# Optimization experiments

Hardware: AMD Instinct MI355X
Metric: run time of the kernel (lower is better)

The kernel has to match this reference:

```python
import jax, jax.numpy as jnp
import numpy as np

VIEW_NUM = 360
CHAN_NUM = 512
BATCH = 2
IMG = 512


def setup_inputs() -> dict:
    key = jax.random.key(0)
    x = jax.random.normal(key, (BATCH, 1, IMG, IMG), dtype=jnp.float32)
    return {"x": x}


def _bilinear_sample_zeros(img, ix, iy):
    """Bilinear sample img (B,1,H,W) at pixel coords ix, iy (H,W), zeros padding.
    Matches F.grid_sample(mode='bilinear', padding_mode='zeros', align_corners=False)."""
    H, W = img.shape[-2], img.shape[-1]
    x0 = jnp.floor(ix)
    y0 = jnp.floor(iy)
    x1 = x0 + 1.0
    y1 = y0 + 1.0
    wx1 = ix - x0
    wx0 = 1.0 - wx1
    wy1 = iy - y0
    wy0 = 1.0 - wy1

    def gather(yy, xx):
        valid = (xx >= 0) & (xx <= W - 1) & (yy >= 0) & (yy <= H - 1)
        xi = jnp.clip(xx, 0, W - 1).astype(jnp.int32)
        yi = jnp.clip(yy, 0, H - 1).astype(jnp.int32)
        # fancy-index over spatial dims -> (B,1,H,W)
        return img[:, :, yi, xi] * valid.astype(img.dtype)

    return (gather(y0, x0) * (wy0 * wx0)
            + gather(y0, x1) * (wy0 * wx1)
            + gather(y1, x0) * (wy1 * wx0)
            + gather(y1, x1) * (wy1 * wx1))


def _fp(x):
    B, C, H, W = x.shape
    # affine_grid base coords, align_corners=False: (2i+1)/N - 1
    bx = (2.0 * jnp.arange(W, dtype=x.dtype) + 1.0) / W - 1.0
    by = (2.0 * jnp.arange(H, dtype=x.dtype) + 1.0) / H - 1.0
    X = bx[None, :]  # (1,W)
    Y = by[:, None]  # (H,1)
    i = jnp.arange(VIEW_NUM, dtype=x.dtype)
    angles = -jnp.pi * (i + 1.0) / VIEW_NUM - jnp.pi
    cosv = jnp.cos(angles)
    sinv = jnp.sin(angles)

    def per_view(carry, cs):
        c, s = cs
        # theta = [[c,-s,0],[s,c,0]]; grid = base @ theta^T
        gx = c * X - s * Y  # (H,W) normalized sample x
        gy = s * X + c * Y  # (H,W) normalized sample y
        # unnormalize (align_corners=False)
        ix = ((gx + 1.0) * W - 1.0) * 0.5
        iy = ((gy + 1.0) * H - 1.0) * 0.5
        samp = _bilinear_sample_zeros(x, ix, iy)  # (B,1,H,W)
        return carry, jnp.sum(samp, axis=2)  # sum over height -> (B,1,W)

    _, cols = jax.lax.scan(per_view, 0, (cosv, sinv))  # (V,B,1,W)
    sino = jnp.transpose(cols, (1, 2, 3, 0)) * 0.5  # (B,1,chanNum,viewNum)
    return sino


def reference(x):
    return _fp(x)
```

## Files before the change

### kernel.cpp

```cpp
#include <hip/hip_runtime.h>

typedef __fp16 h2 __attribute__((ext_vector_type(2)));

constexpr int VIEWS = 360;
constexpr int IMGSZ = 512;
constexpr int BATCH = 2;
constexpr int WCHUNK = 64;
constexpr int KH = 64;
constexpr int NXF4 = 25;
constexpr int PITCH = 100;
constexpr int MAXNY = 94;
constexpr int PW = 712;
constexpr int PH = 704;
constexpr int PAD = 96;

__global__ __launch_bounds__(256) void pad_kernel(const float* __restrict__ x,
                                                  unsigned* __restrict__ padq) {
    constexpr int PW4 = PW / 4;
    constexpr int total = PH * PW4;
    int idx = blockIdx.x * 256 + threadIdx.x;
    if (idx >= total) return;
    int py = idx / PW4;
    int px4 = idx - py * PW4;
    int gx = px4 * 4 - PAD;
    int gy = py - PAD;
    const float* img0 = x;
    const float* img1 = x + (size_t)IMGSZ * IMGSZ;
    bool rowok = (unsigned)gy < (unsigned)IMGSZ;
    float4 a = make_float4(0.f, 0.f, 0.f, 0.f);
    float4 bq = a;
    if (rowok && (unsigned)gx < (unsigned)IMGSZ) {
        a  = *(const float4*)(img0 + (size_t)gy * IMGSZ + gx);
        bq = *(const float4*)(img1 + (size_t)gy * IMGSZ + gx);
    }
    uint4 d;
    d.x = __builtin_bit_cast(unsigned, __builtin_amdgcn_cvt_pkrtz(a.x, bq.x));
    d.y = __builtin_bit_cast(unsigned, __builtin_amdgcn_cvt_pkrtz(a.y, bq.y));
    d.z = __builtin_bit_cast(unsigned, __builtin_amdgcn_cvt_pkrtz(a.z, bq.z));
    d.w = __builtin_bit_cast(unsigned, __builtin_amdgcn_cvt_pkrtz(a.w, bq.w));
    *(uint4*)&padq[(size_t)idx * 4] = d;
}

__global__ __launch_bounds__(256) void fp_kernel(const unsigned* __restrict__ padq,
                                                 float* __restrict__ out) {
    __shared__ __align__(16) unsigned tileU[10240];

    int blk = blockIdx.x;
    int wc = blk & 7;
    int v = blk >> 3;

    int tid = threadIdx.x;
    int lane = tid & 63;
    int g = tid >> 6;
    int w = wc * WCHUNK + lane;

    double ang = -3.14159265358979323846 * (double)(v + 1) / (double)VIEWS
                 - 3.14159265358979323846;
    float c = (float)cos(ang);
    float s = (float)sin(ang);

    float xw = (float)w + 0.5f - 256.0f;
    float cxw = fmaf(c, xw, 255.5f);
    float sxw = fmaf(s, xw, 255.5f);

    float lo = -1e30f, hi = 1e30f;
    {
        float coef = -s, base = cxw;
        if (fabsf(coef) > 1e-6f) {
            float a = (-1.0f - base) / coef;
            float bq = (512.0f - base) / coef;
            lo = fmaxf(lo, fminf(a, bq));
            hi = fminf(hi, fmaxf(a, bq));
        } else if (!(base > -1.0f && base < 512.0f)) {
            lo = 1e30f; hi = -1e30f;
        }
    }
    {
        float coef = c, base = sxw;
        if (fabsf(coef) > 1e-6f) {
            float a = (-1.0f - base) / coef;
            float bq = (512.0f - base) / coef;
            lo = fmaxf(lo, fminf(a, bq));
            hi = fminf(hi, fmaxf(a, bq));
        } else if (!(base > -1.0f && base < 512.0f)) {
            lo = 1e30f; hi = -1e30f;
        }
    }
    float h0f = fminf(fmaxf(floorf(lo + 255.5f) - 1.0f, 0.0f), 512.0f);
    float h1f = fminf(fmaxf(ceilf(hi + 255.5f) + 1.0f, -1.0f), 511.0f);
    int h0 = (int)h0f;
    int h1 = (int)h1f;

    int bh0 = h0, bh1 = h1;
    #pragma unroll
    for (int m = 1; m < 64; m <<= 1) {
        bh0 = min(bh0, __shfl_xor(bh0, m, 64));
        bh1 = max(bh1, __shfl_xor(bh1, m, 64));
    }

    float xa = (float)(wc * WCHUNK) + 0.5f - 256.0f;
    float xb = xa + 63.0f;

    float acc0 = 0.0f, acc1 = 0.0f;
    float step4x = -4.0f * s;
    float step4y = 4.0f * c;

    for (int hc = bh0; hc <= bh1; hc += KH) {
        int hend = min(hc + KH - 1, bh1);

        float ha = (float)hc - 255.5f;
        float hb = (float)hend - 255.5f;
        float ix00 = c * xa - s * ha, ix01 = c * xa - s * hb;
        float ix10 = c * xb - s * ha, ix11 = c * xb - s * hb;
        float iy00 = s * xa + c * ha, iy01 = s * xa + c * hb;
        float iy10 = s * xb + c * ha, iy11 = s * xb + c * hb;
        float ixmn = fminf(fminf(ix00, ix01), fminf(ix10, ix11)) + 255.5f;
        float iymn = fminf(fminf(iy00, iy01), fminf(iy10, iy11)) + 255.5f;
        float iymx = fmaxf(fmaxf(iy00, iy01), fmaxf(iy10, iy11)) + 255.5f;
        int x_lo = (int)floorf(ixmn) - 1;
        int x_lo4 = x_lo & ~3;
        int y_lo = (int)floorf(iymn) - 1;
        int NY = min((int)floorf(iymx) + 3 - y_lo, MAXNY);
        int total4 = NY * NXF4;
        int nit = (total4 + 255) >> 8;

        __syncthreads();

        {
            const unsigned* pb = padq + (y_lo + PAD) * PW + (x_lo4 + PAD);
            for (int k = 0; k < nit; ++k) {
                int i = (k << 8) + tid;
                int ic = min(i, total4 - 1);
                int ry = ic / NXF4;
                uint4 val = *(const uint4*)(pb + 4 * ic + (PW - 4 * NXF4) * ry);
                *(uint4*)&tileU[i << 2] = val;
            }
        }
        __syncthreads();

        float hh0 = (float)(hc + g) - 255.5f;
        float ixr = fmaf(-s, hh0, cxw) - (float)x_lo4;
        float iyr = fmaf(c, hh0, sxw) - (float)y_lo;
        h2 accp0 = (h2)0.0f;
        h2 accp1 = (h2)0.0f;
        int parity = 0;
        #pragma unroll 4
        for (int h = hc + g; h <= hend; h += 4) {
            float fx = floorf(ixr);
            float fy = floorf(iyr);
            int lx = (int)fx;
            int ly = (int)fy;
            float wx1 = ixr - fx;
            float wy1 = iyr - fy;
            h2 wx0s = __builtin_amdgcn_cvt_pkrtz(1.0f - wx1, 1.0f - wx1);
            h2 wx1s = __builtin_amdgcn_cvt_pkrtz(wx1, wx1);
            h2 wy0s = __builtin_amdgcn_cvt_pkrtz(1.0f - wy1, 1.0f - wy1);
            h2 wy1s = __builtin_amdgcn_cvt_pkrtz(wy1, wy1);
            const unsigned* p = tileU + (ly * PITCH + lx);
            unsigned q00 = p[0];
            unsigned q01 = p[1];
            unsigned q10 = p[PITCH];
            unsigned q11 = p[PITCH + 1];
            h2 r0 = __builtin_bit_cast(h2, q00) * wx0s
                  + __builtin_bit_cast(h2, q01) * wx1s;
            h2 r1 = __builtin_bit_cast(h2, q10) * wx0s
                  + __builtin_bit_cast(h2, q11) * wx1s;
            h2 contrib = r0 * wy0s + r1 * wy1s;
            if (parity) accp1 += contrib; else accp0 += contrib;
            parity ^= 1;
            ixr += step4x;
            iyr += step4y;
        }
        acc0 += (float)accp0.x + (float)accp1.x;
        acc1 += (float)accp0.y + (float)accp1.y;
    }

    __syncthreads();
    tileU[(g << 6) + lane] = __float_as_uint(acc0);
    tileU[256 + (g << 6) + lane] = __float_as_uint(acc1);
    __syncthreads();
    if (g == 0) {
        float r0 = __uint_as_float(tileU[lane]) + __uint_as_float(tileU[64 + lane]) +
                   __uint_as_float(tileU[128 + lane]) + __uint_as_float(tileU[192 + lane]);
        float r1 = __uint_as_float(tileU[256 + lane]) + __uint_as_float(tileU[320 + lane]) +
                   __uint_as_float(tileU[384 + lane]) + __uint_as_float(tileU[448 + lane]);
        size_t o = (size_t)w * VIEWS + v;
        out[o] = r0 * 0.5f;
        out[(size_t)IMGSZ * VIEWS + o] = r1 * 0.5f;
    }
}

extern "C" void kernel_launch(void* const* d_in, const int* in_sizes, int n_in,
                              void* d_out, int out_size, void* d_ws, size_t ws_size,
                              hipStream_t stream) {
    const float* x = (const float*)d_in[0];
    float* out = (float*)d_out;
    unsigned* padq = (unsigned*)d_ws;

    constexpr int padTotal = PH * (PW / 4);
    pad_kernel<<<(padTotal + 255) / 256, 256, 0, stream>>>(x, padq);

    int nblocks = VIEWS * (IMGSZ / WCHUNK);
    fp_kernel<<<nblocks, 256, 0, stream>>>(padq, out);
}
```

Measured before the change: 159.6 us.

## Fuse padding/fp16 packing into tile load and shrink tile height

```diff
diff --git a/kernel.cpp b/kernel.cpp
--- a/kernel.cpp
+++ b/kernel.cpp
@@ -4,46 +4,15 @@
 
 constexpr int VIEWS = 360;
 constexpr int IMGSZ = 512;
-constexpr int BATCH = 2;
 constexpr int WCHUNK = 64;
-constexpr int KH = 64;
-constexpr int NXF4 = 25;
-constexpr int PITCH = 100;
-constexpr int MAXNY = 94;
-constexpr int PW = 712;
-constexpr int PH = 704;
-constexpr int PAD = 96;
+constexpr int KH = 32;
+constexpr int NXF4 = 20;
+constexpr int PITCH = 80;
+constexpr int MAXNY = 76;
 
-__global__ __launch_bounds__(256) void pad_kernel(const float* __restrict__ x,
-                                                  unsigned* __restrict__ padq) {
-    constexpr int PW4 = PW / 4;
-    constexpr int total = PH * PW4;
-    int idx = blockIdx.x * 256 + threadIdx.x;
-    if (idx >= total) return;
-    int py = idx / PW4;
-    int px4 = idx - py * PW4;
-    int gx = px4 * 4 - PAD;
-    int gy = py - PAD;
-    const float* img0 = x;
-    const float* img1 = x + (size_t)IMGSZ * IMGSZ;
-    bool rowok = (unsigned)gy < (unsigned)IMGSZ;
-    float4 a = make_float4(0.f, 0.f, 0.f, 0.f);
-    float4 bq = a;
-    if (rowok && (unsigned)gx < (unsigned)IMGSZ) {
-        a  = *(const float4*)(img0 + (size_t)gy * IMGSZ + gx);
-        bq = *(const float4*)(img1 + (size_t)gy * IMGSZ + gx);
-    }
-    uint4 d;
-    d.x = __builtin_bit_cast(unsigned, __builtin_amdgcn_cvt_pkrtz(a.x, bq.x));
-    d.y = __builtin_bit_cast(unsigned, __builtin_amdgcn_cvt_pkrtz(a.y, bq.y));
-    d.z = __builtin_bit_cast(unsigned, __builtin_amdgcn_cvt_pkrtz(a.z, bq.z));
-    d.w = __builtin_bit_cast(unsigned, __builtin_amdgcn_cvt_pkrtz(a.w, bq.w));
-    *(uint4*)&padq[(size_t)idx * 4] = d;
-}
-
-__global__ __launch_bounds__(256) void fp_kernel(const unsigned* __restrict__ padq,
+__global__ __launch_bounds__(256) void fp_kernel(const float* __restrict__ x,
                                                  float* __restrict__ out) {
-    __shared__ __align__(16) unsigned tileU[10240];
+    __shared__ __align__(16) unsigned tileU[6144];
 
     int blk = blockIdx.x;
     int wc = blk & 7;
@@ -58,6 +27,9 @@
                  - 3.14159265358979323846;
     float c = (float)cos(ang);
     float s = (float)sin(ang);
+
+    const float* __restrict__ img0 = x;
+    const float* __restrict__ img1 = x + (size_t)IMGSZ * IMGSZ;
 
     float xw = (float)w + 0.5f - 256.0f;
     float cxw = fmaf(c, xw, 255.5f);
@@ -126,15 +98,28 @@
 
         __syncthreads();
 
-        {
-            const unsigned* pb = padq + (y_lo + PAD) * PW + (x_lo4 + PAD);
-            for (int k = 0; k < nit; ++k) {
-                int i = (k << 8) + tid;
-                int ic = min(i, total4 - 1);
-                int ry = ic / NXF4;
-                uint4 val = *(const uint4*)(pb + 4 * ic + (PW - 4 * NXF4) * ry);
-                *(uint4*)&tileU[i << 2] = val;
+        for (int k = 0; k < nit; ++k) {
+            int i = (k << 8) + tid;
+            int ic = min(i, total4 - 1);
+            int ry = ic / NXF4;
+            int rx4 = ic - ry * NXF4;
+            int gy = y_lo + ry;
+            int gx = x_lo4 + (rx4 << 2);
+            bool ok = ((unsigned)gy < (unsigned)IMGSZ) &
+                      ((unsigned)gx < (unsigned)IMGSZ);
+            float4 a = make_float4(0.f, 0.f, 0.f, 0.f);
+            float4 bq = a;
+            if (ok) {
+                size_t off = (size_t)gy * IMGSZ + gx;
+                a  = *(const float4*)(img0 + off);
+                bq = *(const float4*)(img1 + off);
             }
+            uint4 d;
+            d.x = __builtin_bit_cast(unsigned, __builtin_amdgcn_cvt_pkrtz(a.x, bq.x));
+            d.y = __builtin_bit_cast(unsigned, __builtin_amdgcn_cvt_pkrtz(a.y, bq.y));
+            d.z = __builtin_bit_cast(unsigned, __builtin_amdgcn_cvt_pkrtz(a.z, bq.z));
+            d.w = __builtin_bit_cast(unsigned, __builtin_amdgcn_cvt_pkrtz(a.w, bq.w));
+            *(uint4*)&tileU[i << 2] = d;
         }
         __syncthreads();
 
@@ -152,20 +137,16 @@
             int ly = (int)fy;
             float wx1 = ixr - fx;
             float wy1 = iyr - fy;
-            h2 wx0s = __builtin_amdgcn_cvt_pkrtz(1.0f - wx1, 1.0f - wx1);
-            h2 wx1s = __builtin_amdgcn_cvt_pkrtz(wx1, wx1);
-            h2 wy0s = __builtin_amdgcn_cvt_pkrtz(1.0f - wy1, 1.0f - wy1);
-            h2 wy1s = __builtin_amdgcn_cvt_pkrtz(wy1, wy1);
+            h2 wxs = __builtin_amdgcn_cvt_pkrtz(wx1, wx1);
+            h2 wys = __builtin_amdgcn_cvt_pkrtz(wy1, wy1);
             const unsigned* p = tileU + (ly * PITCH + lx);
-            unsigned q00 = p[0];
-            unsigned q01 = p[1];
-            unsigned q10 = p[PITCH];
-            unsigned q11 = p[PITCH + 1];
-            h2 r0 = __builtin_bit_cast(h2, q00) * wx0s
-                  + __builtin_bit_cast(h2, q01) * wx1s;
-            h2 r1 = __builtin_bit_cast(h2, q10) * wx0s
-                  + __builtin_bit_cast(h2, q11) * wx1s;
-            h2 contrib = r0 * wy0s + r1 * wy1s;
+            h2 t00 = __builtin_bit_cast(h2, p[0]);
+            h2 t01 = __builtin_bit_cast(h2, p[1]);
+            h2 t10 = __builtin_bit_cast(h2, p[PITCH]);
+            h2 t11 = __builtin_bit_cast(h2, p[PITCH + 1]);
+            h2 r0 = t00 + (t01 - t00) * wxs;
+            h2 r1 = t10 + (t11 - t10) * wxs;
+            h2 contrib = r0 + (r1 - r0) * wys;
             if (parity) accp1 += contrib; else accp0 += contrib;
             parity ^= 1;
             ixr += step4x;
@@ -195,11 +176,6 @@
                               hipStream_t stream) {
     const float* x = (const float*)d_in[0];
     float* out = (float*)d_out;
-    unsigned* padq = (unsigned*)d_ws;
-
-    constexpr int padTotal = PH * (PW / 4);
-    pad_kernel<<<(padTotal + 255) / 256, 256, 0, stream>>>(x, padq);
-
     int nblocks = VIEWS * (IMGSZ / WCHUNK);
-    fp_kernel<<<nblocks, 256, 0, stream>>>(padq, out);
+    fp_kernel<<<nblocks, 256, 0, stream>>>(x, out);
 }
```

After: 184.8 us. +15.8%, slower.
